# Kernel tuning notes

Hardware: AMD Instinct MI355X
Metric: run time of the kernel (lower is better)

Reference implementation:

```python
import jax, jax.numpy as jnp
import numpy as np

TEMPERATURE = 0.5
BATCH = 2048  # N = batch_size * world_size (world_size = 1)
FEAT = 128
EPS = 1e-8  # torch CosineSimilarity default eps


def _build_mask_indices(N):
    """Replicates mask_correlated_samples + the row-major boolean gather
    sim[mask].reshape(2N, -1). Returns static flat indices [2N, 2N-1]."""
    sub = np.ones((2 * N, 2 * N), dtype=bool)
    np.fill_diagonal(sub, False)
    idx = np.arange(N)
    sub[idx, N + idx] = False
    sub[N + idx, idx] = False
    mask = np.zeros((3 * N, 3 * N), dtype=bool)
    mask[:2 * N, :2 * N] = sub
    mask[idx, 2 * N + idx] = True
    mask[2 * N + idx, idx] = True
    flat = np.nonzero(mask.ravel())[0]  # row-major order, 2N*(2N-1) entries
    return flat.reshape(2 * N, 2 * N - 1)


_NEG_IDX = jnp.asarray(_build_mask_indices(BATCH), dtype=jnp.int32)


def setup_inputs() -> dict:
    key = jax.random.key(0)
    ka, kp, kn = jax.random.split(key, 3)
    return {
        "anchor": jax.random.normal(ka, (BATCH, FEAT), dtype=jnp.float32),
        "pos": jax.random.normal(kp, (BATCH, FEAT), dtype=jnp.float32),
        "neg": jax.random.normal(kn, (BATCH, FEAT), dtype=jnp.float32),
    }


def reference(anchor, pos, neg):
    N = anchor.shape[0]
    z = jnp.concatenate([anchor, pos, neg], axis=0)  # [3N, d]
    zn = z / jnp.maximum(jnp.linalg.norm(z, axis=1, keepdims=True), EPS)
    sim = (zn @ zn.T) / TEMPERATURE  # [3N, 3N]
    # positive pairs: diagonals at offset +/-2N (anchor<->neg pairs)
    sim_i_j = jnp.diagonal(sim, offset=2 * N)[:N]
    sim_j_i = jnp.diagonal(sim, offset=-2 * N)[:N]
    positive = jnp.concatenate([sim_i_j, sim_j_i]).reshape(2 * N, 1)
    # masked gather of negatives (static index table, row-major order)
    negative = jnp.take(sim.ravel(), _NEG_IDX)  # [2N, 2N-1]
    logits = jnp.concatenate([positive, negative], axis=1)  # [2N, 2N]
    # cross-entropy with label 0, reduction='sum', then / (2N)
    loss = jnp.sum(jax.nn.logsumexp(logits, axis=1) - logits[:, 0]) / (2 * N)
    return loss
```

## Files before the change

### kernel.cpp

```cpp
#include <hip/hip_runtime.h>
#include <hip/hip_bf16.h>

#define N_      2048
#define TWO_N   4096
#define DFEAT   128
#define SCALE   2.0f
#define BROWS   128
#define BCOLS   128
#define NT      (BCOLS / 16)
#define LDSTR   132
#define SC_L2E  2.8853900817779268f

typedef __attribute__((ext_vector_type(8))) short bf16x8;
typedef __attribute__((ext_vector_type(4))) float f32x4;

__global__ __launch_bounds__(256) void k_prep(const float* __restrict__ a,
                                              const float* __restrict__ p,
                                              const float* __restrict__ ng,
                                              __hip_bfloat16* __restrict__ zn16,
                                              float* __restrict__ dvec,
                                              float* __restrict__ accS,
                                              float* __restrict__ accP) {
  const int wave = threadIdx.x >> 6;
  const int lane = threadIdx.x & 63;
  const int row  = blockIdx.x * 4 + wave;

  if (threadIdx.x < 4)        accS[blockIdx.x * 4 + threadIdx.x] = 0.0f;
  else if (threadIdx.x < 6)   accP[blockIdx.x * 2 + threadIdx.x - 4] = 0.0f;

  if (row < N_) {
    float2 u = ((const float2*)(a  + (size_t)row * DFEAT))[lane];
    float2 w = ((const float2*)(ng + (size_t)row * DFEAT))[lane];
    float saa = u.x * u.x + u.y * u.y;
    float snn = w.x * w.x + w.y * w.y;
    float san = u.x * w.x + u.y * w.y;
#pragma unroll
    for (int m = 1; m < 64; m <<= 1) {
      saa += __shfl_xor(saa, m);
      snn += __shfl_xor(snn, m);
      san += __shfl_xor(san, m);
    }
    float na = fmaxf(sqrtf(saa), 1e-8f);
    float rn = 1.0f / na;
    __hip_bfloat162 h;
    h.x = __float2bfloat16(u.x * rn);
    h.y = __float2bfloat16(u.y * rn);
    ((__hip_bfloat162*)zn16)[row * (DFEAT / 2) + lane] = h;
    if (lane == 0)
      dvec[row] = SCALE * san / (na * fmaxf(sqrtf(snn), 1e-8f));
  } else {
    float2 v = ((const float2*)(p + (size_t)(row - N_) * DFEAT))[lane];
    float ss = v.x * v.x + v.y * v.y;
#pragma unroll
    for (int m = 1; m < 64; m <<= 1) ss += __shfl_xor(ss, m);
    float rn = 1.0f / fmaxf(sqrtf(ss), 1e-8f);
    __hip_bfloat162 h;
    h.x = __float2bfloat16(v.x * rn);
    h.y = __float2bfloat16(v.y * rn);
    ((__hip_bfloat162*)zn16)[row * (DFEAT / 2) + lane] = h;
  }
}

__global__ __launch_bounds__(256) void k_simsum(const __hip_bfloat16* __restrict__ zn16,
                                                float* __restrict__ accS,
                                                float* __restrict__ accP) {
  __shared__ __align__(16) short Bp[BCOLS * LDSTR];

  const int bx = blockIdx.x, by = blockIdx.y;
  const int wave = threadIdx.x >> 6;
  const int lane = threadIdx.x & 63;
  const int lr   = lane & 15;
  const int kg   = lane >> 4;
  const int rows_base = bx * BROWS + wave * 32;
  const int cb0 = by * BCOLS;
  const short* zs = (const short*)zn16;

  const bool hi = (bx >= 16);
  const int cls = (by == bx) ? 0
                : (!hi && by == bx + 16) ? 1
                : (hi && by == bx - 16) ? 2
                : (hi && by < bx - 16) ? 3
                : 4;

  bf16x8 a0[4], a1[4];
#pragma unroll
  for (int kk = 0; kk < 4; ++kk) {
    a0[kk] = *(const bf16x8*)(zs + (size_t)(rows_base + lr) * DFEAT + kk * 32 + kg * 8);
    a1[kk] = *(const bf16x8*)(zs + (size_t)(rows_base + 16 + lr) * DFEAT + kk * 32 + kg * 8);
  }

#pragma unroll
  for (int it = 0; it < 8; ++it) {
    const int g   = it * 256 + threadIdx.x;
    const int col = g >> 4;
    const int q   = g & 15;
    bf16x8 v = *(const bf16x8*)(zs + (size_t)(cb0 + col) * DFEAT + q * 8);
    *(bf16x8*)(&Bp[col * LDSTR + q * 8]) = v;
  }
  __syncthreads();

  int rrow[2][4], excl[2][4];
#pragma unroll
  for (int t = 0; t < 2; ++t)
#pragma unroll
    for (int j = 0; j < 4; ++j) {
      rrow[t][j] = rows_base + t * 16 + kg * 4 + j;
      excl[t][j] = (cls == 0) ? rrow[t][j]
                 : (cls == 1) ? rrow[t][j] + N_
                 : (cls == 2) ? rrow[t][j] - N_ : -1;
    }

  float acc1v[2][4] = {{0.f,0.f,0.f,0.f},{0.f,0.f,0.f,0.f}};
  float acc2v[2][4] = {{0.f,0.f,0.f,0.f},{0.f,0.f,0.f,0.f}};

  bf16x8 bcur[4], bnxt[4];
#pragma unroll
  for (int kk = 0; kk < 4; ++kk)
    bcur[kk] = *(const bf16x8*)(&Bp[lr * LDSTR + kk * 32 + kg * 8]);

#pragma unroll 2
  for (int ct = 0; ct < NT; ++ct) {
    const int ctn = (ct + 1 < NT) ? (ct + 1) : ct;
#pragma unroll
    for (int kk = 0; kk < 4; ++kk)
      bnxt[kk] = *(const bf16x8*)(&Bp[(ctn * 16 + lr) * LDSTR + kk * 32 + kg * 8]);

    f32x4 acc0 = {0.f, 0.f, 0.f, 0.f};
    f32x4 acc1 = {0.f, 0.f, 0.f, 0.f};
#pragma unroll
    for (int kk = 0; kk < 4; ++kk) {
      acc0 = __builtin_amdgcn_mfma_f32_16x16x32_bf16(a0[kk], bcur[kk], acc0, 0, 0, 0);
      acc1 = __builtin_amdgcn_mfma_f32_16x16x32_bf16(a1[kk], bcur[kk], acc1, 0, 0, 0);
    }

    const int c = cb0 + ct * 16 + lr;
    if (cls >= 3) {
#pragma unroll
      for (int j = 0; j < 4; ++j) {
        acc1v[0][j] += __builtin_amdgcn_exp2f(acc0[j] * SC_L2E);
        acc1v[1][j] += __builtin_amdgcn_exp2f(acc1[j] * SC_L2E);
      }
    } else if (cls == 2) {
#pragma unroll
      for (int j = 0; j < 4; ++j) {
        float e0 = __builtin_amdgcn_exp2f(acc0[j] * SC_L2E);
        e0 = (c == excl[0][j]) ? 0.0f : e0;
        if (c < excl[0][j]) acc2v[0][j] += e0; else acc1v[0][j] += e0;
        float e1 = __builtin_amdgcn_exp2f(acc1[j] * SC_L2E);
        e1 = (c == excl[1][j]) ? 0.0f : e1;
        if (c < excl[1][j]) acc2v[1][j] += e1; else acc1v[1][j] += e1;
      }
    } else {
#pragma unroll
      for (int j = 0; j < 4; ++j) {
        float e0 = __builtin_amdgcn_exp2f(acc0[j] * SC_L2E);
        acc1v[0][j] += (c == excl[0][j]) ? 0.0f : e0;
        float e1 = __builtin_amdgcn_exp2f(acc1[j] * SC_L2E);
        acc1v[1][j] += (c == excl[1][j]) ? 0.0f : e1;
      }
    }

#pragma unroll
    for (int kk = 0; kk < 4; ++kk) bcur[kk] = bnxt[kk];
  }

#pragma unroll
  for (int t = 0; t < 2; ++t)
#pragma unroll
    for (int j = 0; j < 4; ++j) {
      float v1 = acc1v[t][j], v2 = acc2v[t][j];
#pragma unroll
      for (int m = 1; m < 16; m <<= 1) {
        v1 += __shfl_xor(v1, m);
        if (cls == 2) v2 += __shfl_xor(v2, m);
      }
      if (lr == 0) {
        const int r = rrow[t][j];
        if (cls == 3)      atomicAdd(&accP[r - N_], v1);
        else               atomicAdd(&accS[r], v1);
        if (cls == 2)      atomicAdd(&accP[r - N_], v2);
      }
    }
}

__global__ __launch_bounds__(1024) void k_final(const float* __restrict__ dvec,
                                                const float* __restrict__ accS,
                                                const float* __restrict__ accP,
                                                float* __restrict__ out) {
  __shared__ float Elds[N_];
  __shared__ float red[16];
  const int tid = threadIdx.x;
  float dpart = 0.f;
  for (int i = tid; i < N_; i += 1024) {
    float E = __expf(dvec[i]);
    Elds[i] = E;
    dpart += E;
  }
#pragma unroll
  for (int m = 1; m < 64; m <<= 1) dpart += __shfl_xor(dpart, m);
  const int w = tid >> 6, l = tid & 63;
  if (l == 0) red[w] = dpart;
  __syncthreads();
  float Dsum = 0.f;
#pragma unroll
  for (int k = 0; k < 16; ++k) Dsum += red[k];
  __syncthreads();

  float part = 0.f;
  for (int r = tid; r < TWO_N; r += 1024) {
    float S = accS[r];
    float t;
    if (r < N_) {
      t = logf(2.0f * Elds[r] + S) - dvec[r];
    } else {
      const int i = r - N_;
      const float extra = (i < N_ - 1) ? accP[i + 1] : Dsum;
      t = logf(Elds[i] + S + extra) - dvec[i];
    }
    part += t;
  }
#pragma unroll
  for (int m = 1; m < 64; m <<= 1) part += __shfl_xor(part, m);
  if (l == 0) red[w] = part;
  __syncthreads();
  if (tid == 0) {
    float tot = 0.f;
#pragma unroll
    for (int k = 0; k < 16; ++k) tot += red[k];
    out[0] = tot / (float)TWO_N;
  }
}

extern "C" void kernel_launch(void* const* d_in, const int* in_sizes, int n_in,
                              void* d_out, int out_size, void* d_ws, size_t ws_size,
                              hipStream_t stream) {
  const float* a  = (const float*)d_in[0];
  const float* p  = (const float*)d_in[1];
  const float* ng = (const float*)d_in[2];

  char* ws = (char*)d_ws;
  __hip_bfloat16* zn16 = (__hip_bfloat16*)ws;
  float* dvec = (float*)(ws + (size_t)TWO_N * DFEAT * 2);
  float* accS = dvec + TWO_N;
  float* accP = accS + TWO_N;

  k_prep<<<TWO_N / 4, 256, 0, stream>>>(a, p, ng, zn16, dvec, accS, accP);
  k_simsum<<<dim3(TWO_N / BROWS, TWO_N / BCOLS), 256, 0, stream>>>(zn16, accS, accP);
  k_final<<<1, 1024, 0, stream>>>(dvec, accS, accP, (float*)d_out);
}
```

Measured before the change: 24.00 us.

## Pad atomic accumulators to separate cache lines and stage A rows via LDS

```diff
diff --git a/kernel.cpp b/kernel.cpp
--- a/kernel.cpp
+++ b/kernel.cpp
@@ -9,6 +9,7 @@
 #define BCOLS   128
 #define NT      (BCOLS / 16)
 #define LDSTR   132
+#define PAD     16
 #define SC_L2E  2.8853900817779268f
 
 typedef __attribute__((ext_vector_type(8))) short bf16x8;
@@ -25,8 +26,8 @@
   const int lane = threadIdx.x & 63;
   const int row  = blockIdx.x * 4 + wave;
 
-  if (threadIdx.x < 4)        accS[blockIdx.x * 4 + threadIdx.x] = 0.0f;
-  else if (threadIdx.x < 6)   accP[blockIdx.x * 2 + threadIdx.x - 4] = 0.0f;
+  if (threadIdx.x < 4)        accS[(blockIdx.x * 4 + threadIdx.x) * PAD] = 0.0f;
+  else if (threadIdx.x < 6)   accP[(blockIdx.x * 2 + threadIdx.x - 4) * PAD] = 0.0f;
 
   if (row < N_) {
     float2 u = ((const float2*)(a  + (size_t)row * DFEAT))[lane];
@@ -82,12 +83,23 @@
                 : (hi && by < bx - 16) ? 3
                 : 4;
 
+#pragma unroll
+  for (int it = 0; it < 8; ++it) {
+    const int g   = it * 256 + threadIdx.x;
+    const int r   = g >> 4;
+    const int q   = g & 15;
+    bf16x8 v = *(const bf16x8*)(zs + (size_t)(bx * BROWS + r) * DFEAT + q * 8);
+    *(bf16x8*)(&Bp[r * LDSTR + q * 8]) = v;
+  }
+  __syncthreads();
+
   bf16x8 a0[4], a1[4];
 #pragma unroll
   for (int kk = 0; kk < 4; ++kk) {
-    a0[kk] = *(const bf16x8*)(zs + (size_t)(rows_base + lr) * DFEAT + kk * 32 + kg * 8);
-    a1[kk] = *(const bf16x8*)(zs + (size_t)(rows_base + 16 + lr) * DFEAT + kk * 32 + kg * 8);
-  }
+    a0[kk] = *(const bf16x8*)(&Bp[(wave * 32 + lr) * LDSTR + kk * 32 + kg * 8]);
+    a1[kk] = *(const bf16x8*)(&Bp[(wave * 32 + 16 + lr) * LDSTR + kk * 32 + kg * 8]);
+  }
+  __syncthreads();
 
 #pragma unroll
   for (int it = 0; it < 8; ++it) {
@@ -176,9 +188,9 @@
       }
       if (lr == 0) {
         const int r = rrow[t][j];
-        if (cls == 3)      atomicAdd(&accP[r - N_], v1);
-        else               atomicAdd(&accS[r], v1);
-        if (cls == 2)      atomicAdd(&accP[r - N_], v2);
+        if (cls == 3)      atomicAdd(&accP[(r - N_) * PAD], v1);
+        else               atomicAdd(&accS[r * PAD], v1);
+        if (cls == 2)      atomicAdd(&accP[(r - N_) * PAD], v2);
       }
     }
 }
@@ -208,13 +220,13 @@
 
   float part = 0.f;
   for (int r = tid; r < TWO_N; r += 1024) {
-    float S = accS[r];
+    float S = accS[r * PAD];
     float t;
     if (r < N_) {
       t = logf(2.0f * Elds[r] + S) - dvec[r];
     } else {
       const int i = r - N_;
-      const float extra = (i < N_ - 1) ? accP[i + 1] : Dsum;
+      const float extra = (i < N_ - 1) ? accP[(i + 1) * PAD] : Dsum;
       t = logf(Elds[i] + S + extra) - dvec[i];
     }
     part += t;
@@ -242,7 +254,7 @@
   __hip_bfloat16* zn16 = (__hip_bfloat16*)ws;
   float* dvec = (float*)(ws + (size_t)TWO_N * DFEAT * 2);
   float* accS = dvec + TWO_N;
-  float* accP = accS + TWO_N;
+  float* accP = accS + TWO_N * PAD;
 
   k_prep<<<TWO_N / 4, 256, 0, stream>>>(a, p, ng, zn16, dvec, accS, accP);
   k_simsum<<<dim3(TWO_N / BROWS, TWO_N / BCOLS), 256, 0, stream>>>(zn16, accS, accP);
```

After: 28.15 us. 17.3% more time.

## Use 256-row similarity tiles, pack prep rows per half-wave, precompute Dsum partials

Applied to the files above, without the earlier changes.

```diff
diff --git a/kernel.cpp b/kernel.cpp
--- a/kernel.cpp
+++ b/kernel.cpp
@@ -5,14 +5,20 @@
 #define TWO_N   4096
 #define DFEAT   128
 #define SCALE   2.0f
-#define BROWS   128
+#define BROWS   256
 #define BCOLS   128
 #define NT      (BCOLS / 16)
 #define LDSTR   132
 #define SC_L2E  2.8853900817779268f
 
 typedef __attribute__((ext_vector_type(8))) short bf16x8;
+typedef __attribute__((ext_vector_type(4))) short short4v;
 typedef __attribute__((ext_vector_type(4))) float f32x4;
+
+static __device__ __forceinline__ short f2bf(float x) {
+  __hip_bfloat16 b = __float2bfloat16(x);
+  return *reinterpret_cast<short*>(&b);
+}
 
 __global__ __launch_bounds__(256) void k_prep(const float* __restrict__ a,
                                               const float* __restrict__ p,
@@ -20,48 +26,59 @@
                                               __hip_bfloat16* __restrict__ zn16,
                                               float* __restrict__ dvec,
                                               float* __restrict__ accS,
-                                              float* __restrict__ accP) {
+                                              float* __restrict__ accP,
+                                              float* __restrict__ DsumPart) {
+  __shared__ float eacc[8];
   const int wave = threadIdx.x >> 6;
   const int lane = threadIdx.x & 63;
-  const int row  = blockIdx.x * 4 + wave;
-
-  if (threadIdx.x < 4)        accS[blockIdx.x * 4 + threadIdx.x] = 0.0f;
-  else if (threadIdx.x < 6)   accP[blockIdx.x * 2 + threadIdx.x - 4] = 0.0f;
-
-  if (row < N_) {
-    float2 u = ((const float2*)(a  + (size_t)row * DFEAT))[lane];
-    float2 w = ((const float2*)(ng + (size_t)row * DFEAT))[lane];
-    float saa = u.x * u.x + u.y * u.y;
-    float snn = w.x * w.x + w.y * w.y;
-    float san = u.x * w.x + u.y * w.y;
-#pragma unroll
-    for (int m = 1; m < 64; m <<= 1) {
+  const int half = lane >> 5;
+  const int sub  = lane & 31;
+  const int row  = blockIdx.x * 8 + wave * 2 + half;
+
+  if (threadIdx.x < 8)        accS[blockIdx.x * 8 + threadIdx.x] = 0.0f;
+  else if (threadIdx.x < 12)  accP[blockIdx.x * 4 + threadIdx.x - 8] = 0.0f;
+
+  const bool lo = (row < N_);
+  if (lo) {
+    float4 u = ((const float4*)(a  + (size_t)row * DFEAT))[sub];
+    float4 w = ((const float4*)(ng + (size_t)row * DFEAT))[sub];
+    float saa = u.x*u.x + u.y*u.y + u.z*u.z + u.w*u.w;
+    float snn = w.x*w.x + w.y*w.y + w.z*w.z + w.w*w.w;
+    float san = u.x*w.x + u.y*w.y + u.z*w.z + u.w*w.w;
+#pragma unroll
+    for (int m = 1; m < 32; m <<= 1) {
       saa += __shfl_xor(saa, m);
       snn += __shfl_xor(snn, m);
       san += __shfl_xor(san, m);
     }
     float na = fmaxf(sqrtf(saa), 1e-8f);
     float rn = 1.0f / na;
-    __hip_bfloat162 h;
-    h.x = __float2bfloat16(u.x * rn);
-    h.y = __float2bfloat16(u.y * rn);
-    ((__hip_bfloat162*)zn16)[row * (DFEAT / 2) + lane] = h;
-    if (lane == 0)
-      dvec[row] = SCALE * san / (na * fmaxf(sqrtf(snn), 1e-8f));
+    short4v h = { f2bf(u.x*rn), f2bf(u.y*rn), f2bf(u.z*rn), f2bf(u.w*rn) };
+    ((short4v*)zn16)[row * (DFEAT/4) + sub] = h;
+    if (sub == 0) {
+      float dv = SCALE * san / (na * fmaxf(sqrtf(snn), 1e-8f));
+      dvec[row] = dv;
+      eacc[wave * 2 + half] = __expf(dv);
+    }
+    __syncthreads();
+    if (threadIdx.x == 0) {
+      float s = 0.f;
+#pragma unroll
+      for (int k = 0; k < 8; ++k) s += eacc[k];
+      DsumPart[blockIdx.x] = s;
+    }
   } else {
-    float2 v = ((const float2*)(p + (size_t)(row - N_) * DFEAT))[lane];
-    float ss = v.x * v.x + v.y * v.y;
-#pragma unroll
-    for (int m = 1; m < 64; m <<= 1) ss += __shfl_xor(ss, m);
+    float4 v = ((const float4*)(p + (size_t)(row - N_) * DFEAT))[sub];
+    float ss = v.x*v.x + v.y*v.y + v.z*v.z + v.w*v.w;
+#pragma unroll
+    for (int m = 1; m < 32; m <<= 1) ss += __shfl_xor(ss, m);
     float rn = 1.0f / fmaxf(sqrtf(ss), 1e-8f);
-    __hip_bfloat162 h;
-    h.x = __float2bfloat16(v.x * rn);
-    h.y = __float2bfloat16(v.y * rn);
-    ((__hip_bfloat162*)zn16)[row * (DFEAT / 2) + lane] = h;
-  }
-}
-
-__global__ __launch_bounds__(256) void k_simsum(const __hip_bfloat16* __restrict__ zn16,
+    short4v h = { f2bf(v.x*rn), f2bf(v.y*rn), f2bf(v.z*rn), f2bf(v.w*rn) };
+    ((short4v*)zn16)[row * (DFEAT/4) + sub] = h;
+  }
+}
+
+__global__ __launch_bounds__(512) void k_simsum(const __hip_bfloat16* __restrict__ zn16,
                                                 float* __restrict__ accS,
                                                 float* __restrict__ accP) {
   __shared__ __align__(16) short Bp[BCOLS * LDSTR];
@@ -75,11 +92,11 @@
   const int cb0 = by * BCOLS;
   const short* zs = (const short*)zn16;
 
-  const bool hi = (bx >= 16);
-  const int cls = (by == bx) ? 0
-                : (!hi && by == bx + 16) ? 1
-                : (hi && by == bx - 16) ? 2
-                : (hi && by < bx - 16) ? 3
+  const bool hi = (bx >= 8);
+  const int cls = (by == 2*bx || by == 2*bx + 1) ? 0
+                : (!hi && (by == 2*bx + 16 || by == 2*bx + 17)) ? 1
+                : (hi && (by == 2*bx - 16 || by == 2*bx - 15)) ? 2
+                : (hi && by < 2*bx - 16) ? 3
                 : 4;
 
   bf16x8 a0[4], a1[4];
@@ -90,8 +107,8 @@
   }
 
 #pragma unroll
-  for (int it = 0; it < 8; ++it) {
-    const int g   = it * 256 + threadIdx.x;
+  for (int it = 0; it < 4; ++it) {
+    const int g   = it * 512 + threadIdx.x;
     const int col = g >> 4;
     const int q   = g & 15;
     bf16x8 v = *(const bf16x8*)(zs + (size_t)(cb0 + col) * DFEAT + q * 8);
@@ -186,38 +203,36 @@
 __global__ __launch_bounds__(1024) void k_final(const float* __restrict__ dvec,
                                                 const float* __restrict__ accS,
                                                 const float* __restrict__ accP,
+                                                const float* __restrict__ DsumPart,
                                                 float* __restrict__ out) {
-  __shared__ float Elds[N_];
   __shared__ float red[16];
   const int tid = threadIdx.x;
-  float dpart = 0.f;
-  for (int i = tid; i < N_; i += 1024) {
-    float E = __expf(dvec[i]);
-    Elds[i] = E;
-    dpart += E;
-  }
-#pragma unroll
-  for (int m = 1; m < 64; m <<= 1) dpart += __shfl_xor(dpart, m);
   const int w = tid >> 6, l = tid & 63;
-  if (l == 0) red[w] = dpart;
+
+  float dval = (tid < 256) ? DsumPart[tid] : 0.0f;
+#pragma unroll
+  for (int m = 1; m < 64; m <<= 1) dval += __shfl_xor(dval, m);
+  if (l == 0) red[w] = dval;
   __syncthreads();
   float Dsum = 0.f;
 #pragma unroll
   for (int k = 0; k < 16; ++k) Dsum += red[k];
   __syncthreads();
 
+  const f32x4 S4 = ((const f32x4*)accS)[tid];
   float part = 0.f;
-  for (int r = tid; r < TWO_N; r += 1024) {
-    float S = accS[r];
-    float t;
+#pragma unroll
+  for (int j = 0; j < 4; ++j) {
+    const int r = tid * 4 + j;
+    const float S = S4[j];
     if (r < N_) {
-      t = logf(2.0f * Elds[r] + S) - dvec[r];
+      part += __logf(2.0f * __expf(dvec[r]) + S) - dvec[r];
     } else {
       const int i = r - N_;
       const float extra = (i < N_ - 1) ? accP[i + 1] : Dsum;
-      t = logf(Elds[i] + S + extra) - dvec[i];
-    }
-    part += t;
+      const float dv = dvec[i];
+      part += __logf(__expf(dv) + S + extra) - dv;
+    }
   }
 #pragma unroll
   for (int m = 1; m < 64; m <<= 1) part += __shfl_xor(part, m);
@@ -243,8 +258,9 @@
   float* dvec = (float*)(ws + (size_t)TWO_N * DFEAT * 2);
   float* accS = dvec + TWO_N;
   float* accP = accS + TWO_N;
-
-  k_prep<<<TWO_N / 4, 256, 0, stream>>>(a, p, ng, zn16, dvec, accS, accP);
-  k_simsum<<<dim3(TWO_N / BROWS, TWO_N / BCOLS), 256, 0, stream>>>(zn16, accS, accP);
-  k_final<<<1, 1024, 0, stream>>>(dvec, accS, accP, (float*)d_out);
-}
+  float* DsumPart = accP + N_;
+
+  k_prep<<<TWO_N / 8, 256, 0, stream>>>(a, p, ng, zn16, dvec, accS, accP, DsumPart);
+  k_simsum<<<dim3(TWO_N / BROWS, TWO_N / BCOLS), 512, 0, stream>>>(zn16, accS, accP);
+  k_final<<<1, 1024, 0, stream>>>(dvec, accS, accP, DsumPart, (float*)d_out);
+}
```

Measured after the change: 24.79 us. 3.3% more time.
